# Kernel tuning notes

Measured on AMD Instinct MI355X. Metric: run time of the kernel, lower is better.

Reference implementation:

```python
import jax, jax.numpy as jnp
import numpy as np

DIMS = 2048
HEAD_DIM = 64
NUM_HEADS = DIMS // HEAD_DIM   # 32
GQA_HEADS = 2                  # KV heads
EPS = 1e-8


def setup_inputs() -> dict:
    key = jax.random.key(0)
    ks = jax.random.split(key, 6)
    b, s = 2, 2048
    kv_dims = HEAD_DIM * GQA_HEADS  # 128
    x = jax.random.normal(ks[0], (b, s, DIMS), dtype=jnp.float32)
    Wq = jax.random.normal(ks[1], (DIMS, DIMS), dtype=jnp.float32) * 0.02
    Wk = jax.random.normal(ks[2], (kv_dims, DIMS), dtype=jnp.float32) * 0.02
    Wv = jax.random.normal(ks[3], (kv_dims, DIMS), dtype=jnp.float32) * 0.02
    Wo = jax.random.normal(ks[4], (DIMS, DIMS), dtype=jnp.float32) * 0.02
    norm_scale = jnp.ones((DIMS,), dtype=jnp.float32)           # RMSNorm.scale
    split_scale = jnp.full((DIMS,), 0.1, dtype=jnp.float32)     # RMS_split.scale
    return {"x": x, "norm_scale": norm_scale, "split_scale": split_scale,
            "Wq": Wq, "Wk": Wk, "Wv": Wv, "Wo": Wo}


def reference(x, norm_scale, split_scale, Wq, Wk, Wv, Wo):
    b, s, d = x.shape
    H, G, dh = NUM_HEADS, GQA_HEADS, HEAD_DIM
    hpg = H // G  # query heads per KV group

    # RMS_split pre-norm: RMSNorm (l2-norm based) then elementwise scale
    nrm = jnp.linalg.norm(x, axis=-1, keepdims=True) * (d ** -0.5)
    h = (norm_scale * x / (nrm + EPS)) * split_scale

    # projections (nn.Linear with weight [out, in], no bias)
    q = (h @ Wq.T).reshape(b, s, H, dh)          # b s H dh
    k = (h @ Wk.T).reshape(b, s, G, dh)          # b s G dh
    v = (h @ Wv.T).reshape(b, s, G, dh)

    # group query heads: b G hpg s dh
    q = q.transpose(0, 2, 1, 3).reshape(b, G, hpg, s, dh)
    k = k.transpose(0, 2, 1, 3)                  # b G s dh
    v = v.transpose(0, 2, 1, 3)                  # b G s dh

    scores = jnp.einsum('bghsd,bgtd->bghst', q, k) / np.float32(np.sqrt(dh))
    attn = jax.nn.softmax(scores, axis=-1)
    out = jnp.einsum('bghst,bgtd->bghsd', attn, v)   # b G hpg s dh

    out = out.reshape(b, H, s, dh).transpose(0, 2, 1, 3).reshape(b, s, H * dh)
    return x + out @ Wo.T
```

## Files before the change

kernel.cpp:

```cpp
#include <hip/hip_runtime.h>

typedef unsigned short u16;
typedef unsigned int u32;
typedef __bf16 bf16x8 __attribute__((ext_vector_type(8)));
typedef float f32x4 __attribute__((ext_vector_type(4)));

#define DIMS 2048
#define SEQ 2048
#define BATCH 2
#define NH 32
#define NG 2
#define DH 64
#define MROWS (BATCH * SEQ)
#define KVD (NG * DH)

#define SCL2 (0.125f * 1.44269504088896f)

__device__ __forceinline__ u16 f2bf(float f) {
  u32 u = __float_as_uint(f);
  u32 r = u + 0x7fffu + ((u >> 16) & 1u);
  return (u16)(r >> 16);
}
__device__ __forceinline__ u32 pack2(float a, float b) {
  return (u32)f2bf(a) | ((u32)f2bf(b) << 16);
}
__device__ __forceinline__ u32 cvtpk(float a, float b) {
#if __has_builtin(__builtin_amdgcn_cvt_pk_bf16_f32)
  typedef __bf16 bf16x2 __attribute__((ext_vector_type(2)));
  union {
    bf16x2 v;
    u32 u;
  } r;
  r.v = __builtin_amdgcn_cvt_pk_bf16_f32(a, b);
  return r.u;
#else
  return pack2(a, b);
#endif
}
__device__ __forceinline__ void glds16(const u16* g, u16* l) {
  __builtin_amdgcn_global_load_lds(
      (const __attribute__((address_space(1))) void*)g,
      (__attribute__((address_space(3))) void*)l, 16, 0, 0);
}

__global__ __launch_bounds__(256) void rms_split_kernel(
    const float* __restrict__ x, const float* __restrict__ ns,
    const float* __restrict__ ss, u16* __restrict__ h) {
  const int row = blockIdx.x;
  const int tid = threadIdx.x;
  const float* xr = x + (size_t)row * DIMS;
  float4 v0 = ((const float4*)xr)[tid];
  float4 v1 = ((const float4*)xr)[tid + 256];
  float s = v0.x * v0.x + v0.y * v0.y + v0.z * v0.z + v0.w * v0.w +
            v1.x * v1.x + v1.y * v1.y + v1.z * v1.z + v1.w * v1.w;
#pragma unroll
  for (int d = 1; d < 64; d <<= 1) s += __shfl_xor(s, d, 64);
  __shared__ float red[4];
  if ((tid & 63) == 0) red[tid >> 6] = s;
  __syncthreads();
  float tot = red[0] + red[1] + red[2] + red[3];
  float inv = 1.0f / (sqrtf(tot * (1.0f / DIMS)) + 1e-8f);
  float4 a0 = ((const float4*)ns)[tid];
  float4 a1 = ((const float4*)ns)[tid + 256];
  float4 b0 = ((const float4*)ss)[tid];
  float4 b1 = ((const float4*)ss)[tid + 256];
  uint2 o0, o1;
  o0.x = pack2(v0.x * a0.x * b0.x * inv, v0.y * a0.y * b0.y * inv);
  o0.y = pack2(v0.z * a0.z * b0.z * inv, v0.w * a0.w * b0.w * inv);
  o1.x = pack2(v1.x * a1.x * b1.x * inv, v1.y * a1.y * b1.y * inv);
  o1.y = pack2(v1.z * a1.z * b1.z * inv, v1.w * a1.w * b1.w * inv);
  uint2* hr = (uint2*)(h + (size_t)row * DIMS);
  hr[tid] = o0;
  hr[tid + 256] = o1;
}

__global__ __launch_bounds__(256) void cvt2_kernel(const float* __restrict__ a,
                                                   u16* __restrict__ oa,
                                                   const float* __restrict__ b,
                                                   u16* __restrict__ ob,
                                                   int half) {
  const int bx = blockIdx.x;
  const float* src = bx < half ? a : b;
  u16* dst = bx < half ? oa : ob;
  const int i = (bx < half ? bx : bx - half) * 256 + threadIdx.x;
  float4 v = ((const float4*)src)[i];
  uint2 r;
  r.x = pack2(v.x, v.y);
  r.y = pack2(v.z, v.w);
  ((uint2*)dst)[i] = r;
}

template <int MODE>
__global__ __launch_bounds__(256) void gemm_bt(
    const u16* __restrict__ A, const u16* __restrict__ B, void* __restrict__ Cv,
    const float* __restrict__ R, u16* __restrict__ kb, u16* __restrict__ vtb,
    int M, int N, int K) {
  __shared__ u16 As[128 * 32];
  __shared__ u16 Bs[128 * 32];
  const int tid = threadIdx.x;
  const int lane = tid & 63;
  const int wv = tid >> 6;
  const int fr = lane & 15;
  const int fq = lane >> 4;
  const int m0 = blockIdx.y * 128;
  const int n0 = blockIdx.x * 128;
  const int wm = wv & 1;
  const int wn = wv >> 1;

  const int srow = tid >> 2;
  const int scol = (tid & 3) * 8;
  const u16* Ag0 = A + (size_t)(m0 + srow) * K + scol;
  const u16* Ag1 = A + (size_t)(m0 + srow + 64) * K + scol;
  const u16* Bg0 = B + (size_t)(n0 + srow) * K + scol;
  const u16* Bg1 = B + (size_t)(n0 + srow + 64) * K + scol;
  u16* Al0 = As + wv * 512;
  u16* Al1 = As + 2048 + wv * 512;
  u16* Bl0 = Bs + wv * 512;
  u16* Bl1 = Bs + 2048 + wv * 512;

  f32x4 acc[4][4];
#pragma unroll
  for (int i = 0; i < 4; ++i)
#pragma unroll
    for (int j = 0; j < 4; ++j)
#pragma unroll
      for (int e = 0; e < 4; ++e) acc[i][j][e] = 0.0f;

  const u16* ap[4];
  const u16* bp[4];
#pragma unroll
  for (int i = 0; i < 4; ++i) {
    ap[i] = As + (wm * 64 + i * 16 + fr) * 32 + fq * 8;
    bp[i] = Bs + (wn * 64 + i * 16 + fr) * 32 + fq * 8;
  }

  for (int k0 = 0; k0 < K; k0 += 32) {
    glds16(Ag0 + k0, Al0);
    glds16(Ag1 + k0, Al1);
    glds16(Bg0 + k0, Bl0);
    glds16(Bg1 + k0, Bl1);
    __syncthreads();
    bf16x8 af[4], bf[4];
#pragma unroll
    for (int i = 0; i < 4; ++i) {
      af[i] = *(const bf16x8*)ap[i];
      bf[i] = *(const bf16x8*)bp[i];
    }
#pragma unroll
    for (int i = 0; i < 4; ++i)
#pragma unroll
      for (int j = 0; j < 4; ++j)
        acc[i][j] = __builtin_amdgcn_mfma_f32_16x16x32_bf16(af[i], bf[j],
                                                            acc[i][j], 0, 0, 0);
    __syncthreads();
  }

#pragma unroll
  for (int i = 0; i < 4; ++i) {
    const int m = m0 + wm * 64 + i * 16 + fq * 4;
#pragma unroll
    for (int j = 0; j < 4; ++j) {
      const int n = n0 + wn * 64 + j * 16 + fr;
#pragma unroll
      for (int r = 0; r < 4; ++r) {
        if (MODE == 1) {
          const size_t idx = (size_t)(m + r) * N + n;
          ((float*)Cv)[idx] = R[idx] + acc[i][j][r];
        } else {
          if (n0 < 2048)
            ((u16*)Cv)[(size_t)(m + r) * DIMS + n] = f2bf(acc[i][j][r]);
          else if (n0 < 2176)
            kb[(size_t)(m + r) * KVD + (n - 2048)] = f2bf(acc[i][j][r] * SCL2);
          else
            vtb[(size_t)(n - 2176) * MROWS + (m + r)] = f2bf(acc[i][j][r]);
        }
      }
    }
  }
}

__global__ __launch_bounds__(128, 2) void attn_kernel(
    const u16* __restrict__ q, const u16* __restrict__ kbuf,
    const u16* __restrict__ vT, u16* __restrict__ out) {
  __shared__ u16 Ks[8 * 512];
  __shared__ u16 Vs[8 * 512];
  const int tid = threadIdx.x;
  const int lane = tid & 63;
  const int wv = tid >> 6;
  const int fr = lane & 15;
  const int fq = lane >> 4;
  const int b = blockIdx.x >> 5;
  const int hq = blockIdx.x & 31;
  const int g = hq >> 4;
  const int q0 = blockIdx.y * 128 + wv * 64;

  bf16x8 af[4][2];
#pragma unroll
  for (int mt = 0; mt < 4; ++mt)
#pragma unroll
    for (int kx = 0; kx < 2; ++kx)
      af[mt][kx] =
          *(const bf16x8*)(q + (size_t)(b * SEQ + q0 + mt * 16 + fr) * DIMS +
                           hq * DH + kx * 32 + fq * 8);

  f32x4 Oa[4][4];
  float lacc[4] = {0.0f, 0.0f, 0.0f, 0.0f};
#pragma unroll
  for (int mt = 0; mt < 4; ++mt)
#pragma unroll
    for (int j = 0; j < 4; ++j)
#pragma unroll
      for (int e = 0; e < 4; ++e) Oa[mt][j][e] = 0.0f;

  const int kk =
      (lane & 32) | ((lane & 16) >> 2) | ((lane & 12) << 1) | (lane & 3);
  const u16* ksrc = kbuf + (size_t)(b * SEQ + kk) * KVD + g * DH;
  const u16* vsrc = vT + (size_t)(g * DH + lane) * MROWS + b * SEQ;

  for (int t0 = 0; t0 < SEQ; t0 += 64) {
#pragma unroll
    for (int s = 0; s < 4; ++s) {
      const int c = wv * 4 + s;
      glds16(ksrc + (size_t)t0 * KVD + (c >> 2) * 32 + (c & 3) * 8,
             Ks + c * 512);
      glds16(vsrc + t0 + c * 8, Vs + c * 512);
    }
    __syncthreads();

#pragma unroll
    for (int kg = 0; kg < 2; ++kg) {
      bf16x8 kf00 = *(const bf16x8*)(Ks + fq * 512 + (kg * 32 + fr) * 8);
      bf16x8 kf01 = *(const bf16x8*)(Ks + (4 + fq) * 512 + (kg * 32 + fr) * 8);
      bf16x8 kf10 = *(const bf16x8*)(Ks + fq * 512 + (kg * 32 + 16 + fr) * 8);
      bf16x8 kf11 =
          *(const bf16x8*)(Ks + (4 + fq) * 512 + (kg * 32 + 16 + fr) * 8);
      bf16x8 vf[4];
#pragma unroll
      for (int jt = 0; jt < 4; ++jt)
        vf[jt] =
            *(const bf16x8*)(Vs + (kg * 4 + fq) * 512 + (jt * 16 + fr) * 8);
#pragma unroll
      for (int mt = 0; mt < 4; ++mt) {
        f32x4 s0 = {0.0f, 0.0f, 0.0f, 0.0f};
        f32x4 s1 = {0.0f, 0.0f, 0.0f, 0.0f};
        s0 = __builtin_amdgcn_mfma_f32_16x16x32_bf16(kf00, af[mt][0], s0, 0, 0, 0);
        s0 = __builtin_amdgcn_mfma_f32_16x16x32_bf16(kf01, af[mt][1], s0, 0, 0, 0);
        s1 = __builtin_amdgcn_mfma_f32_16x16x32_bf16(kf10, af[mt][0], s1, 0, 0, 0);
        s1 = __builtin_amdgcn_mfma_f32_16x16x32_bf16(kf11, af[mt][1], s1, 0, 0, 0);
        const float p0 = __builtin_amdgcn_exp2f(s0[0]);
        const float p1 = __builtin_amdgcn_exp2f(s0[1]);
        const float p2 = __builtin_amdgcn_exp2f(s0[2]);
        const float p3 = __builtin_amdgcn_exp2f(s0[3]);
        const float p4 = __builtin_amdgcn_exp2f(s1[0]);
        const float p5 = __builtin_amdgcn_exp2f(s1[1]);
        const float p6 = __builtin_amdgcn_exp2f(s1[2]);
        const float p7 = __builtin_amdgcn_exp2f(s1[3]);
        lacc[mt] += ((p0 + p1) + (p2 + p3)) + ((p4 + p5) + (p6 + p7));
        union {
          bf16x8 v;
          u32 u[4];
        } pu;
        pu.u[0] = cvtpk(p0, p1);
        pu.u[1] = cvtpk(p2, p3);
        pu.u[2] = cvtpk(p4, p5);
        pu.u[3] = cvtpk(p6, p7);
#pragma unroll
        for (int jt = 0; jt < 4; ++jt)
          Oa[mt][jt] =
              __builtin_amdgcn_mfma_f32_16x16x32_bf16(pu.v, vf[jt], Oa[mt][jt], 0, 0, 0);
      }
    }
    __syncthreads();
  }

#pragma unroll
  for (int mt = 0; mt < 4; ++mt) {
    float l = lacc[mt];
    l += __shfl_xor(l, 16, 64);
    l += __shfl_xor(l, 32, 64);
    lacc[mt] = l;
  }
#pragma unroll
  for (int mt = 0; mt < 4; ++mt)
#pragma unroll
    for (int r = 0; r < 4; ++r) {
      const float invl = 1.0f / __shfl(lacc[mt], fq * 4 + r, 64);
      const int row = q0 + mt * 16 + fq * 4 + r;
#pragma unroll
      for (int jt = 0; jt < 4; ++jt)
        out[(size_t)(b * SEQ + row) * DIMS + hq * DH + jt * 16 + fr] =
            f2bf(Oa[mt][jt][r] * invl);
    }
}

extern "C" void kernel_launch(void* const* d_in, const int* in_sizes, int n_in,
                              void* d_out, int out_size, void* d_ws,
                              size_t ws_size, hipStream_t stream) {
  const float* x = (const float*)d_in[0];
  const float* ns = (const float*)d_in[1];
  const float* ssc = (const float*)d_in[2];
  const float* Wq = (const float*)d_in[3];
  const float* Wk = (const float*)d_in[4];
  const float* Wv = (const float*)d_in[5];
  const float* Wo = (const float*)d_in[6];

  char* ws = (char*)d_ws;
  u16* hbuf = (u16*)(ws);
  u16* bqkv = (u16*)(ws + 16777216);
  u16* bWo = (u16*)(ws + 26214400);
  u16* qb = (u16*)(ws + 34603008);
  u16* kb = (u16*)(ws + 51380224);
  u16* vtb = (u16*)(ws + 52428800);
  u16* ab = (u16*)(ws + 53477376);

  rms_split_kernel<<<dim3(4096), dim3(256), 0, stream>>>(x, ns, ssc, hbuf);
  cvt2_kernel<<<dim3(8192), dim3(256), 0, stream>>>(Wq, bqkv, Wo, bWo, 4096);
  cvt2_kernel<<<dim3(512), dim3(256), 0, stream>>>(
      Wk, bqkv + (size_t)2048 * 2048, Wv, bqkv + (size_t)2176 * 2048, 256);

  gemm_bt<2><<<dim3(18, 32), dim3(256), 0, stream>>>(
      hbuf, bqkv, qb, nullptr, kb, vtb, 4096, 2048, 2048);
  attn_kernel<<<dim3(64, 16), dim3(128), 0, stream>>>(qb, kb, vtb, ab);
  gemm_bt<1><<<dim3(16, 32), dim3(256), 0, stream>>>(
      ab, bWo, d_out, x, nullptr, nullptr, 4096, 2048, 2048);
}
```

Baseline: 354.4 us.

## Double-buffer K/V tiles in attention, 4 waves per block, MFMA row sums

Attention blocks grow from 2 to 4 waves (256 queries per block), so each K/V tile is shared by more query rows. K/V tiles are double-buffered in LDS and the next tile is prefetched with manual vmcnt waits and barriers, overlapping global loads with MFMA work. The softmax denominator is now accumulated by an extra MFMA against a vector of ones instead of scalar adds plus cross-lane shuffles. In exchange, each wave issues one more MFMA per 16-row tile, the block uses twice the LDS, and the hand-written waitcnt scheme relies on a fixed count of outstanding loads.

```diff
diff --git a/kernel.cpp b/kernel.cpp
--- a/kernel.cpp
+++ b/kernel.cpp
@@ -179,11 +179,11 @@
   }
 }
 
-__global__ __launch_bounds__(128, 2) void attn_kernel(
+__global__ __launch_bounds__(256, 2) void attn_kernel(
     const u16* __restrict__ q, const u16* __restrict__ kbuf,
     const u16* __restrict__ vT, u16* __restrict__ out) {
-  __shared__ u16 Ks[8 * 512];
-  __shared__ u16 Vs[8 * 512];
+  __shared__ u16 Ks[2][8 * 512];
+  __shared__ u16 Vs[2][8 * 512];
   const int tid = threadIdx.x;
   const int lane = tid & 63;
   const int wv = tid >> 6;
@@ -192,7 +192,7 @@
   const int b = blockIdx.x >> 5;
   const int hq = blockIdx.x & 31;
   const int g = hq >> 4;
-  const int q0 = blockIdx.y * 128 + wv * 64;
+  const int q0 = blockIdx.y * 256 + wv * 64;
 
   bf16x8 af[4][2];
 #pragma unroll
@@ -204,87 +204,106 @@
                            hq * DH + kx * 32 + fq * 8);
 
   f32x4 Oa[4][4];
-  float lacc[4] = {0.0f, 0.0f, 0.0f, 0.0f};
-#pragma unroll
-  for (int mt = 0; mt < 4; ++mt)
+  f32x4 On[4];
+#pragma unroll
+  for (int mt = 0; mt < 4; ++mt) {
+#pragma unroll
+    for (int e = 0; e < 4; ++e) On[mt][e] = 0.0f;
 #pragma unroll
     for (int j = 0; j < 4; ++j)
 #pragma unroll
       for (int e = 0; e < 4; ++e) Oa[mt][j][e] = 0.0f;
+  }
+
+  bf16x8 onev;
+#pragma unroll
+  for (int e = 0; e < 8; ++e) onev[e] = (__bf16)1.0f;
 
   const int kk =
       (lane & 32) | ((lane & 16) >> 2) | ((lane & 12) << 1) | (lane & 3);
   const u16* ksrc = kbuf + (size_t)(b * SEQ + kk) * KVD + g * DH;
   const u16* vsrc = vT + (size_t)(g * DH + lane) * MROWS + b * SEQ;
 
-  for (int t0 = 0; t0 < SEQ; t0 += 64) {
-#pragma unroll
-    for (int s = 0; s < 4; ++s) {
-      const int c = wv * 4 + s;
-      glds16(ksrc + (size_t)t0 * KVD + (c >> 2) * 32 + (c & 3) * 8,
-             Ks + c * 512);
-      glds16(vsrc + t0 + c * 8, Vs + c * 512);
-    }
-    __syncthreads();
-
-#pragma unroll
-    for (int kg = 0; kg < 2; ++kg) {
-      bf16x8 kf00 = *(const bf16x8*)(Ks + fq * 512 + (kg * 32 + fr) * 8);
-      bf16x8 kf01 = *(const bf16x8*)(Ks + (4 + fq) * 512 + (kg * 32 + fr) * 8);
-      bf16x8 kf10 = *(const bf16x8*)(Ks + fq * 512 + (kg * 32 + 16 + fr) * 8);
-      bf16x8 kf11 =
-          *(const bf16x8*)(Ks + (4 + fq) * 512 + (kg * 32 + 16 + fr) * 8);
-      bf16x8 vf[4];
-#pragma unroll
-      for (int jt = 0; jt < 4; ++jt)
-        vf[jt] =
-            *(const bf16x8*)(Vs + (kg * 4 + fq) * 512 + (jt * 16 + fr) * 8);
-#pragma unroll
-      for (int mt = 0; mt < 4; ++mt) {
-        f32x4 s0 = {0.0f, 0.0f, 0.0f, 0.0f};
-        f32x4 s1 = {0.0f, 0.0f, 0.0f, 0.0f};
-        s0 = __builtin_amdgcn_mfma_f32_16x16x32_bf16(kf00, af[mt][0], s0, 0, 0, 0);
-        s0 = __builtin_amdgcn_mfma_f32_16x16x32_bf16(kf01, af[mt][1], s0, 0, 0, 0);
-        s1 = __builtin_amdgcn_mfma_f32_16x16x32_bf16(kf10, af[mt][0], s1, 0, 0, 0);
-        s1 = __builtin_amdgcn_mfma_f32_16x16x32_bf16(kf11, af[mt][1], s1, 0, 0, 0);
-        const float p0 = __builtin_amdgcn_exp2f(s0[0]);
-        const float p1 = __builtin_amdgcn_exp2f(s0[1]);
-        const float p2 = __builtin_amdgcn_exp2f(s0[2]);
-        const float p3 = __builtin_amdgcn_exp2f(s0[3]);
-        const float p4 = __builtin_amdgcn_exp2f(s1[0]);
-        const float p5 = __builtin_amdgcn_exp2f(s1[1]);
-        const float p6 = __builtin_amdgcn_exp2f(s1[2]);
-        const float p7 = __builtin_amdgcn_exp2f(s1[3]);
-        lacc[mt] += ((p0 + p1) + (p2 + p3)) + ((p4 + p5) + (p6 + p7));
-        union {
-          bf16x8 v;
-          u32 u[4];
-        } pu;
-        pu.u[0] = cvtpk(p0, p1);
-        pu.u[1] = cvtpk(p2, p3);
-        pu.u[2] = cvtpk(p4, p5);
-        pu.u[3] = cvtpk(p6, p7);
-#pragma unroll
-        for (int jt = 0; jt < 4; ++jt)
-          Oa[mt][jt] =
-              __builtin_amdgcn_mfma_f32_16x16x32_bf16(pu.v, vf[jt], Oa[mt][jt], 0, 0, 0);
-      }
-    }
-    __syncthreads();
-  }
-
-#pragma unroll
-  for (int mt = 0; mt < 4; ++mt) {
-    float l = lacc[mt];
-    l += __shfl_xor(l, 16, 64);
-    l += __shfl_xor(l, 32, 64);
-    lacc[mt] = l;
-  }
+  const int c0 = wv * 2;
+#define STAGE(buf, tile)                                                     \
+  {                                                                          \
+    const int t0_ = (tile)*64;                                               \
+    _Pragma("unroll") for (int s = 0; s < 2; ++s) {                          \
+      const int c = c0 + s;                                                  \
+      glds16(ksrc + (size_t)t0_ * KVD + (c >> 2) * 32 + (c & 3) * 8,         \
+             &Ks[buf][c * 512]);                                             \
+      glds16(vsrc + t0_ + c * 8, &Vs[buf][c * 512]);                         \
+    }                                                                        \
+  }
+
+#define COMPUTE(buf)                                                          \
+  {                                                                           \
+    _Pragma("unroll") for (int kg = 0; kg < 2; ++kg) {                        \
+      bf16x8 kf00 = *(const bf16x8*)(&Ks[buf][fq * 512 + (kg * 32 + fr) * 8]); \
+      bf16x8 kf01 =                                                           \
+          *(const bf16x8*)(&Ks[buf][(4 + fq) * 512 + (kg * 32 + fr) * 8]);    \
+      bf16x8 kf10 =                                                           \
+          *(const bf16x8*)(&Ks[buf][fq * 512 + (kg * 32 + 16 + fr) * 8]);     \
+      bf16x8 kf11 = *(const bf16x8*)(&Ks[buf][(4 + fq) * 512 +                \
+                                              (kg * 32 + 16 + fr) * 8]);      \
+      bf16x8 vf[4];                                                           \
+      _Pragma("unroll") for (int jt = 0; jt < 4; ++jt) vf[jt] =               \
+          *(const bf16x8*)(&Vs[buf][(kg * 4 + fq) * 512 + (jt * 16 + fr) * 8]); \
+      _Pragma("unroll") for (int mt = 0; mt < 4; ++mt) {                      \
+        f32x4 s0 = {0.0f, 0.0f, 0.0f, 0.0f};                                  \
+        f32x4 s1 = {0.0f, 0.0f, 0.0f, 0.0f};                                  \
+        s0 = __builtin_amdgcn_mfma_f32_16x16x32_bf16(kf00, af[mt][0], s0, 0,  \
+                                                     0, 0);                   \
+        s0 = __builtin_amdgcn_mfma_f32_16x16x32_bf16(kf01, af[mt][1], s0, 0,  \
+                                                     0, 0);                   \
+        s1 = __builtin_amdgcn_mfma_f32_16x16x32_bf16(kf10, af[mt][0], s1, 0,  \
+                                                     0, 0);                   \
+        s1 = __builtin_amdgcn_mfma_f32_16x16x32_bf16(kf11, af[mt][1], s1, 0,  \
+                                                     0, 0);                   \
+        const float p0 = __builtin_amdgcn_exp2f(s0[0]);                       \
+        const float p1 = __builtin_amdgcn_exp2f(s0[1]);                       \
+        const float p2 = __builtin_amdgcn_exp2f(s0[2]);                       \
+        const float p3 = __builtin_amdgcn_exp2f(s0[3]);                       \
+        const float p4 = __builtin_amdgcn_exp2f(s1[0]);                       \
+        const float p5 = __builtin_amdgcn_exp2f(s1[1]);                       \
+        const float p6 = __builtin_amdgcn_exp2f(s1[2]);                       \
+        const float p7 = __builtin_amdgcn_exp2f(s1[3]);                       \
+        union {                                                               \
+          bf16x8 v;                                                           \
+          u32 u[4];                                                           \
+        } pu;                                                                 \
+        pu.u[0] = cvtpk(p0, p1);                                              \
+        pu.u[1] = cvtpk(p2, p3);                                              \
+        pu.u[2] = cvtpk(p4, p5);                                              \
+        pu.u[3] = cvtpk(p6, p7);                                              \
+        _Pragma("unroll") for (int jt = 0; jt < 4; ++jt) Oa[mt][jt] =         \
+            __builtin_amdgcn_mfma_f32_16x16x32_bf16(pu.v, vf[jt], Oa[mt][jt], \
+                                                    0, 0, 0);                 \
+        On[mt] = __builtin_amdgcn_mfma_f32_16x16x32_bf16(pu.v, onev, On[mt],  \
+                                                         0, 0, 0);            \
+      }                                                                       \
+    }                                                                         \
+  }
+
+  STAGE(0, 0);
+  for (int it = 0; it < 32; it += 2) {
+    STAGE(1, (it + 1) & 31);
+    asm volatile("s_waitcnt vmcnt(4)\ns_barrier" ::: "memory");
+    COMPUTE(0);
+    asm volatile("s_barrier" ::: "memory");
+    STAGE(0, (it + 2) & 31);
+    asm volatile("s_waitcnt vmcnt(4)\ns_barrier" ::: "memory");
+    COMPUTE(1);
+    asm volatile("s_barrier" ::: "memory");
+  }
+#undef STAGE
+#undef COMPUTE
+
 #pragma unroll
   for (int mt = 0; mt < 4; ++mt)
 #pragma unroll
     for (int r = 0; r < 4; ++r) {
-      const float invl = 1.0f / __shfl(lacc[mt], fq * 4 + r, 64);
+      const float invl = 1.0f / On[mt][r];
       const int row = q0 + mt * 16 + fq * 4 + r;
 #pragma unroll
       for (int jt = 0; jt < 4; ++jt)
@@ -320,7 +339,7 @@
 
   gemm_bt<2><<<dim3(18, 32), dim3(256), 0, stream>>>(
       hbuf, bqkv, qb, nullptr, kb, vtb, 4096, 2048, 2048);
-  attn_kernel<<<dim3(64, 16), dim3(128), 0, stream>>>(qb, kb, vtb, ab);
+  attn_kernel<<<dim3(64, 8), dim3(256), 0, stream>>>(qb, kb, vtb, ab);
   gemm_bt<1><<<dim3(16, 32), dim3(256), 0, stream>>>(
       ab, bWo, d_out, x, nullptr, nullptr, 4096, 2048, 2048);
 }
```

Result: faster. 339.5 us (-4.2%).
